# Optimization experiments

Measured on AMD Instinct MI355X. Metric: run time of the kernel, lower is better.

Reference implementation:

```python
import jax, jax.numpy as jnp
import numpy as np

N = 10000      # cells (nodes)
F_IN = 512     # genes (features)
H = 40         # hidden_dim
DEG = 16       # avg kNN degree
EPS = 1e-5     # GraphNorm eps


def gcn(x, W, b, src, dst, coef):
    # PyG GCNConv: transform then symmetric-normalized aggregate (+bias)
    h = x @ W                                   # [N, out]
    msg = h[src] * coef[:, None]                # [E, out]
    out = jax.ops.segment_sum(msg, dst, num_segments=N)
    return out + b


def graph_norm(x, weight, bias, alpha):
    # PyG GraphNorm over a single graph: mean/var across nodes, learnable mean scale
    mean = jnp.mean(x, axis=0, keepdims=True)
    shifted = x - alpha * mean
    var = jnp.mean(shifted * shifted, axis=0, keepdims=True)
    return weight * shifted * jax.lax.rsqrt(var + EPS) + bias


def setup_inputs() -> dict:
    key = jax.random.key(0)
    ks = jax.random.split(key, 8)
    x = jax.random.uniform(ks[0], (N, F_IN), dtype=jnp.float32)
    E = N * DEG
    src = jax.random.randint(ks[1], (E,), 0, N)
    dst = jax.random.randint(ks[2], (E,), 0, N)
    loop = jnp.arange(N)
    src = jnp.concatenate([src, loop])          # add self-loops (GCNConv default)
    dst = jnp.concatenate([dst, loop])

    def glorot(k, shape):
        lim = np.sqrt(6.0 / (shape[0] + shape[1])).astype(np.float32)
        return jax.random.uniform(k, shape, jnp.float32, -lim, lim)

    W1 = glorot(ks[3], (F_IN, H)); b1 = jnp.zeros((H,), jnp.float32)
    gn_w = jnp.ones((H,), jnp.float32)
    gn_b = jnp.zeros((H,), jnp.float32)
    gn_a = jnp.ones((H,), jnp.float32)          # mean_scale alpha
    Wm = glorot(ks[4], (H, F_IN)); bm = jnp.zeros((F_IN,), jnp.float32)
    Wd = glorot(ks[5], (H, F_IN)); bd = jnp.zeros((F_IN,), jnp.float32)
    Wp = glorot(ks[6], (H, F_IN)); bp = jnp.zeros((F_IN,), jnp.float32)
    return {"x": x, "src": src, "dst": dst, "W1": W1, "b1": b1,
            "gn_w": gn_w, "gn_b": gn_b, "gn_a": gn_a,
            "Wm": Wm, "bm": bm, "Wd": Wd, "bd": bd, "Wp": Wp, "bp": bp}


def reference(x, src, dst, W1, b1, gn_w, gn_b, gn_a, Wm, bm, Wd, bd, Wp, bp):
    # symmetric GCN normalization (self-loops already in edge list, so deg >= 1)
    deg = jax.ops.segment_sum(jnp.ones_like(src, dtype=x.dtype), dst, num_segments=N)
    dis = jax.lax.rsqrt(deg)
    coef = dis[src] * dis[dst]                  # [E]

    hidden = jax.nn.relu(graph_norm(gcn(x, W1, b1, src, dst, coef), gn_w, gn_b, gn_a))
    # Dropout(0.3) is identity at inference
    _mean = jnp.clip(jnp.exp(gcn(hidden, Wm, bm, src, dst, coef)), 1e-5, 1e6)
    _disp = jnp.clip(jax.nn.softplus(gcn(hidden, Wd, bd, src, dst, coef)), 1e-4, 1e4)
    _pi = jax.nn.sigmoid(gcn(hidden, Wp, bp, src, dst, coef))
    return (_mean, _disp, _pi)
```

## Files before the change

### kernel.cpp

```cpp
#include <hip/hip_runtime.h>
#include <math.h>

#define NN 10000
#define FIN 512
#define HD 40
#define GEPS 1e-5f

#define ZI4 ((2 * NN + 2 * HD) / 4)
#define MM1_BLOCKS ((NN + 15) / 16)
#define ZERO_BLOCKS ((ZI4 + 255) / 256)
#define CVT_BLOCKS ((3 * 32 * 3 * 64 + 255) / 256)

typedef _Float16 h4 __attribute__((ext_vector_type(4)));
typedef float f4 __attribute__((ext_vector_type(4)));

__global__ void k_hist(const int* __restrict__ dst, int* __restrict__ cnt, int E) {
    int e = blockIdx.x * blockDim.x + threadIdx.x;
    if (e < E) atomicAdd(&cnt[dst[e]], 1);
}

__global__ __launch_bounds__(1024) void k_scan(const int* __restrict__ cnt,
                                               int* __restrict__ rowstart,
                                               float* __restrict__ dis) {
    __shared__ int lds[1024];
    const int t = threadIdx.x;
    const int start = t * 16;
    int4 c[4];
    int s = 0;
    if (start < NN) {
#pragma unroll
        for (int q = 0; q < 4; ++q) {
            c[q] = *(const int4*)(cnt + start + q * 4);
            s += c[q].x + c[q].y + c[q].z + c[q].w;
        }
    }
    lds[t] = s;
    __syncthreads();
    for (int off = 1; off < 1024; off <<= 1) {
        int v = (t >= off) ? lds[t - off] : 0;
        __syncthreads();
        lds[t] += v;
        __syncthreads();
    }
    if (start < NN) {
        int run = lds[t] - s;
#pragma unroll
        for (int q = 0; q < 4; ++q) {
            int4 rs; float4 dv;
            rs.x = run; dv.x = rsqrtf((float)c[q].x); run += c[q].x;
            rs.y = run; dv.y = rsqrtf((float)c[q].y); run += c[q].y;
            rs.z = run; dv.z = rsqrtf((float)c[q].z); run += c[q].z;
            rs.w = run; dv.w = rsqrtf((float)c[q].w); run += c[q].w;
            *(int4*)(rowstart + start + q * 4) = rs;
            *(float4*)(dis + start + q * 4) = dv;
        }
        if (start + 16 == NN) rowstart[NN] = run;
    }
}

__global__ void k_fill(const int* __restrict__ src, const int* __restrict__ dst,
                       const int* __restrict__ rowstart, int* __restrict__ cur,
                       const float* __restrict__ dis, int2* __restrict__ csr, int E) {
    int e = blockIdx.x * blockDim.x + threadIdx.x;
    if (e >= E) return;
    int s = src[e], d = dst[e];
    int pos = rowstart[d] + atomicAdd(&cur[d], 1);
    int2 v;
    v.x = s;
    v.y = __float_as_int(dis[s] * dis[d]);
    csr[pos] = v;
}

__global__ __launch_bounds__(256) void k_mm1z(const float* __restrict__ x,
                                              const float* __restrict__ W1,
                                              float* __restrict__ h1,
                                              int4* __restrict__ zbuf,
                                              const float* __restrict__ Wm,
                                              const float* __restrict__ Wd,
                                              const float* __restrict__ Wp,
                                              _Float16* __restrict__ Whf) {
    if (blockIdx.x >= MM1_BLOCKS + ZERO_BLOCKS) {
        int idx = (blockIdx.x - MM1_BLOCKS - ZERO_BLOCKS) * 256 + threadIdx.x;
        if (idx < 3 * 32 * 3 * 64) {
            int lane = idx & 63;
            int kk   = (idx >> 6) % 3;
            int ct   = ((idx >> 6) / 3) % 32;
            int z    = idx / (64 * 3 * 32);
            const float* W = (z == 0) ? Wm : (z == 1) ? Wd : Wp;
            int col = ct * 16 + (lane & 15);
            h4 v;
#pragma unroll
            for (int j = 0; j < 4; ++j) {
                int krow = kk * 16 + (lane >> 4) * 4 + j;
                v[j] = (krow < HD) ? (_Float16)W[(size_t)krow * FIN + col] : (_Float16)0.f;
            }
            *(h4*)(Whf + (size_t)idx * 4) = v;
        }
        return;
    }
    if (blockIdx.x >= MM1_BLOCKS) {
        int i = (blockIdx.x - MM1_BLOCKS) * 256 + threadIdx.x;
        if (i < ZI4) zbuf[i] = make_int4(0, 0, 0, 0);
        return;
    }
    __shared__ float red[256 * 41];
    const int tid = threadIdx.x;
    const int r = tid & 15;
    const int kg = tid >> 4;
    const int row = blockIdx.x * 16 + r;
    const int rowc = min(row, NN - 1);
    const float4* xr = (const float4*)(x + (size_t)rowc * FIN + kg * 32);
    float acc[HD];
#pragma unroll
    for (int c = 0; c < HD; ++c) acc[c] = 0.f;
#pragma unroll 2
    for (int q = 0; q < 8; ++q) {
        float4 xv = xr[q];
        const float* wbase = W1 + (size_t)(kg * 32 + q * 4) * HD;
#pragma unroll
        for (int kk = 0; kk < 4; ++kk) {
            float xs = (kk == 0) ? xv.x : (kk == 1) ? xv.y : (kk == 2) ? xv.z : xv.w;
#pragma unroll
            for (int c4 = 0; c4 < 10; ++c4) {
                float4 wv = *(const float4*)(wbase + kk * HD + c4 * 4);
                acc[c4 * 4 + 0] = fmaf(xs, wv.x, acc[c4 * 4 + 0]);
                acc[c4 * 4 + 1] = fmaf(xs, wv.y, acc[c4 * 4 + 1]);
                acc[c4 * 4 + 2] = fmaf(xs, wv.z, acc[c4 * 4 + 2]);
                acc[c4 * 4 + 3] = fmaf(xs, wv.w, acc[c4 * 4 + 3]);
            }
        }
    }
#pragma unroll
    for (int c = 0; c < HD; ++c) red[tid * 41 + c] = acc[c];
    __syncthreads();
    if (tid < 160) {
        int rr = tid / 10, c4 = tid % 10;
        float o0 = 0.f, o1 = 0.f, o2 = 0.f, o3 = 0.f;
#pragma unroll
        for (int kg2 = 0; kg2 < 16; ++kg2) {
            const float* p = &red[(kg2 * 16 + rr) * 41 + c4 * 4];
            o0 += p[0]; o1 += p[1]; o2 += p[2]; o3 += p[3];
        }
        int orow = blockIdx.x * 16 + rr;
        if (orow < NN)
            *(float4*)&h1[(size_t)orow * HD + c4 * 4] = make_float4(o0, o1, o2, o3);
    }
}

template <bool NORM>
__global__ __launch_bounds__(256) void k_gather(const int* __restrict__ rowstart,
                                                const int2* __restrict__ csr,
                                                const float* __restrict__ hin,
                                                const float* __restrict__ stats,
                                                const float* __restrict__ b1,
                                                const float* __restrict__ gw,
                                                const float* __restrict__ gb,
                                                const float* __restrict__ ga,
                                                float* __restrict__ aggout_f,
                                                _Float16* __restrict__ aggout_h) {
    __shared__ float4 part[256];
    __shared__ float csc[2 * HD];
    const int t = threadIdx.x;
    if (NORM) {
        if (t < HD) {
            float m   = stats[t] * (1.0f / NN);
            float ex2 = stats[HD + t] * (1.0f / NN);
            float a   = ga[t];
            float var = ex2 - 2.0f * a * m * m + a * a * m * m;
            float sc  = gw[t] * rsqrtf(var + GEPS);
            csc[t]      = sc;
            csc[HD + t] = sc * (b1[t] - a * m) + gb[t];
        }
        __syncthreads();
    }
    const int slot = blockIdx.x * 128 + (t & 127);
    const int half = t >> 7;
    float4 acc = make_float4(0.f, 0.f, 0.f, 0.f);
    if (slot < NN * 10) {
        const int n = slot / 10, c4 = slot % 10;
        const int j0 = rowstart[n], j1 = rowstart[n + 1];
        const int mid = j0 + ((j1 - j0 + 1) >> 1);
        const int ja = half ? mid : j0;
        const int jb = half ? j1 : mid;
        float4 sc, sh;
        if (NORM) {
            sc = ((const float4*)csc)[c4];
            sh = ((const float4*)csc)[10 + c4];
        }
        for (int j = ja; j < jb; j += 8) {
            const int jm = jb - 1;
            int2 e[8];
#pragma unroll
            for (int q = 0; q < 8; ++q) e[q] = csr[min(j + q, jm)];
            float4 v[8];
#pragma unroll
            for (int q = 0; q < 8; ++q)
                v[q] = *(const float4*)&hin[(size_t)e[q].x * HD + c4 * 4];
#pragma unroll
            for (int q = 0; q < 8; ++q) {
                float cf = (j + q < jb) ? __int_as_float(e[q].y) : 0.f;
                if (NORM) {
                    v[q].x = fmaxf(fmaf(sc.x, v[q].x, sh.x), 0.f);
                    v[q].y = fmaxf(fmaf(sc.y, v[q].y, sh.y), 0.f);
                    v[q].z = fmaxf(fmaf(sc.z, v[q].z, sh.z), 0.f);
                    v[q].w = fmaxf(fmaf(sc.w, v[q].w, sh.w), 0.f);
                }
                acc.x = fmaf(v[q].x, cf, acc.x);
                acc.y = fmaf(v[q].y, cf, acc.y);
                acc.z = fmaf(v[q].z, cf, acc.z);
                acc.w = fmaf(v[q].w, cf, acc.w);
            }
        }
    }
    part[t] = acc;
    __syncthreads();
    if (half == 0 && slot < NN * 10) {
        const int n = slot / 10, c4 = slot % 10;
        float4 p2 = part[t + 128];
        acc.x += p2.x; acc.y += p2.y; acc.z += p2.z; acc.w += p2.w;
        if (NORM) {
            h4 hv = { (_Float16)acc.x, (_Float16)acc.y, (_Float16)acc.z, (_Float16)acc.w };
            *(h4*)(aggout_h + (size_t)n * 48 + c4 * 4) = hv;
            if (c4 == 0) {
                h4 zv = { (_Float16)0.f, (_Float16)0.f, (_Float16)0.f, (_Float16)0.f };
                *(h4*)(aggout_h + (size_t)n * 48 + 40) = zv;
                *(h4*)(aggout_h + (size_t)n * 48 + 44) = zv;
            }
        } else {
            ((float4*)aggout_f)[slot] = acc;
        }
    }
}

__global__ __launch_bounds__(256) void k_stats(const float* __restrict__ agg1,
                                               const float* __restrict__ b1,
                                               float* __restrict__ stats) {
    __shared__ float s0[HD], s1[HD];
    if (threadIdx.x < HD) { s0[threadIdx.x] = 0.f; s1[threadIdx.x] = 0.f; }
    __syncthreads();
    const int gid = blockIdx.x * 256 + threadIdx.x;
    const int c4 = gid % 10;
    float4 bv = ((const float4*)b1)[c4];
    float4 a0 = make_float4(0.f, 0.f, 0.f, 0.f);
    float4 a1 = a0;
    for (int i4 = gid; i4 < NN * 10; i4 += 80 * 256) {
        float4 v = ((const float4*)agg1)[i4];
        v.x += bv.x; v.y += bv.y; v.z += bv.z; v.w += bv.w;
        a0.x += v.x; a0.y += v.y; a0.z += v.z; a0.w += v.w;
        a1.x = fmaf(v.x, v.x, a1.x);
        a1.y = fmaf(v.y, v.y, a1.y);
        a1.z = fmaf(v.z, v.z, a1.z);
        a1.w = fmaf(v.w, v.w, a1.w);
    }
    atomicAdd(&s0[c4 * 4 + 0], a0.x); atomicAdd(&s0[c4 * 4 + 1], a0.y);
    atomicAdd(&s0[c4 * 4 + 2], a0.z); atomicAdd(&s0[c4 * 4 + 3], a0.w);
    atomicAdd(&s1[c4 * 4 + 0], a1.x); atomicAdd(&s1[c4 * 4 + 1], a1.y);
    atomicAdd(&s1[c4 * 4 + 2], a1.z); atomicAdd(&s1[c4 * 4 + 3], a1.w);
    __syncthreads();
    if (threadIdx.x < HD) {
        atomicAdd(&stats[threadIdx.x], s0[threadIdx.x]);
        atomicAdd(&stats[HD + threadIdx.x], s1[threadIdx.x]);
    }
}

__device__ __forceinline__ float activate_rt(float z, int act) {
    if (act == 0) {
        return fminf(fmaxf(__expf(z), 1e-5f), 1e6f);
    } else if (act == 1) {
        float sp = fmaxf(z, 0.0f) + __logf(1.0f + __expf(-fabsf(z)));
        return fminf(fmaxf(sp, 1e-4f), 1e4f);
    }
    return __fdividef(1.0f, 1.0f + __expf(-z));
}

__global__ __launch_bounds__(256) void k_heads3m(const _Float16* __restrict__ agghh,
                                                 const _Float16* __restrict__ Whf,
                                                 const float* __restrict__ bm,
                                                 const float* __restrict__ bd,
                                                 const float* __restrict__ bp,
                                                 float* __restrict__ out) {
    const int z = blockIdx.z;
    const float* bias = (z == 0) ? bm : (z == 1) ? bd : bp;
    float* o = out + (size_t)z * NN * FIN;

    const int lane = threadIdx.x & 63;
    const int wv   = threadIdx.x >> 6;
    const int rowbase = blockIdx.x * 16;
    const int r16  = lane & 15;
    const int kgrp = lane >> 4;

    const _Float16* arow = agghh + (size_t)(rowbase + r16) * 48 + kgrp * 4;
    h4 g0 = *(const h4*)(arow);
    h4 g1 = *(const h4*)(arow + 16);
    h4 g2 = *(const h4*)(arow + 32);

    const int grow = rowbase + r16;
    float* orow = o + (size_t)grow * FIN;

#pragma unroll
    for (int i = 0; i < 8; ++i) {
        const int ct = wv * 8 + i;
        const _Float16* wb = Whf + ((size_t)(z * 32 + ct) * 3) * 256 + lane * 4;
        h4 w0 = *(const h4*)(wb);
        h4 w1 = *(const h4*)(wb + 256);
        h4 w2 = *(const h4*)(wb + 512);
        f4 acc = {0.f, 0.f, 0.f, 0.f};
        acc = __builtin_amdgcn_mfma_f32_16x16x16f16(w0, g0, acc, 0, 0, 0);
        acc = __builtin_amdgcn_mfma_f32_16x16x16f16(w1, g1, acc, 0, 0, 0);
        acc = __builtin_amdgcn_mfma_f32_16x16x16f16(w2, g2, acc, 0, 0, 0);
        const int col0 = ct * 16 + kgrp * 4;
        float4 bv = *(const float4*)&bias[col0];
        float4 ov;
        ov.x = activate_rt(acc[0] + bv.x, z);
        ov.y = activate_rt(acc[1] + bv.y, z);
        ov.z = activate_rt(acc[2] + bv.z, z);
        ov.w = activate_rt(acc[3] + bv.w, z);
        *(float4*)(orow + col0) = ov;
    }
}

extern "C" void kernel_launch(void* const* d_in, const int* in_sizes, int n_in,
                              void* d_out, int out_size, void* d_ws, size_t ws_size,
                              hipStream_t stream) {
    const float* x   = (const float*)d_in[0];
    const int*   src = (const int*)d_in[1];
    const int*   dst = (const int*)d_in[2];
    const float* W1  = (const float*)d_in[3];
    const float* b1  = (const float*)d_in[4];
    const float* gnw = (const float*)d_in[5];
    const float* gnb = (const float*)d_in[6];
    const float* gna = (const float*)d_in[7];
    const float* Wm  = (const float*)d_in[8];
    const float* bm  = (const float*)d_in[9];
    const float* Wd  = (const float*)d_in[10];
    const float* bd  = (const float*)d_in[11];
    const float* Wp  = (const float*)d_in[12];
    const float* bp  = (const float*)d_in[13];
    const int E = in_sizes[1];

    float*     ws       = (float*)d_ws;
    float*     h1       = ws;
    float*     agg1     = h1 + (size_t)NN * HD;
    int*       cnt      = (int*)(agg1 + (size_t)NN * HD);
    int*       cur      = cnt + NN;
    float*     stats    = (float*)(cur + NN);
    float*     dis      = stats + 2 * HD;
    int*       rowstart = (int*)(dis + NN);
    int2*      csr      = (int2*)(rowstart + NN + 2);
    _Float16*  Whf      = (_Float16*)(csr + E);
    _Float16*  agghh    = (_Float16*)h1;
    float*     out      = (float*)d_out;

    k_mm1z<<<MM1_BLOCKS + ZERO_BLOCKS + CVT_BLOCKS, 256, 0, stream>>>(
        x, W1, h1, (int4*)cnt, Wm, Wd, Wp, Whf);
    k_hist<<<(E + 255) / 256, 256, 0, stream>>>(dst, cnt, E);
    k_scan<<<1, 1024, 0, stream>>>(cnt, rowstart, dis);
    k_fill<<<(E + 255) / 256, 256, 0, stream>>>(src, dst, rowstart, cur, dis, csr, E);
    const int gblocks = (NN * 10 + 127) / 128;
    k_gather<false><<<gblocks, 256, 0, stream>>>(rowstart, csr, h1, nullptr,
                                                 nullptr, nullptr, nullptr, nullptr,
                                                 agg1, nullptr);
    k_stats<<<80, 256, 0, stream>>>(agg1, b1, stats);
    k_gather<true><<<gblocks, 256, 0, stream>>>(rowstart, csr, agg1, stats,
                                                b1, gnw, gnb, gna,
                                                nullptr, agghh);
    dim3 hgrid(MM1_BLOCKS, 1, 3);
    k_heads3m<<<hgrid, 256, 0, stream>>>(agghh, Whf, bm, bd, bp, out);
}
```

Before: 110.3 us.

## Fuse GraphNorm stats into first gather and second gather into heads GEMM

Folds the column sum and sum-of-squares reduction into the first aggregation kernel using LDS atomics, removing the separate stats pass over agg1. It also merges the normalized second aggregation with the three MFMA output heads: each 512-thread block gathers 16 rows into shared fp16 and then computes all three heads for them. This removes two launches and the global round trip of the fp16 hidden buffer. In exchange, the gather phase runs on only 320 of 512 threads, the grid has far fewer blocks, and the stats kernel now does many more shared atomics.

```diff
diff --git a/kernel.cpp b/kernel.cpp
--- a/kernel.cpp
+++ b/kernel.cpp
@@ -147,32 +147,17 @@
     }
 }
 
-template <bool NORM>
-__global__ __launch_bounds__(256) void k_gather(const int* __restrict__ rowstart,
-                                                const int2* __restrict__ csr,
-                                                const float* __restrict__ hin,
-                                                const float* __restrict__ stats,
-                                                const float* __restrict__ b1,
-                                                const float* __restrict__ gw,
-                                                const float* __restrict__ gb,
-                                                const float* __restrict__ ga,
-                                                float* __restrict__ aggout_f,
-                                                _Float16* __restrict__ aggout_h) {
+__global__ __launch_bounds__(256) void k_gather1s(const int* __restrict__ rowstart,
+                                                  const int2* __restrict__ csr,
+                                                  const float* __restrict__ hin,
+                                                  const float* __restrict__ b1,
+                                                  float* __restrict__ agg1,
+                                                  float* __restrict__ stats) {
     __shared__ float4 part[256];
-    __shared__ float csc[2 * HD];
+    __shared__ float s0[HD], s1[HD];
     const int t = threadIdx.x;
-    if (NORM) {
-        if (t < HD) {
-            float m   = stats[t] * (1.0f / NN);
-            float ex2 = stats[HD + t] * (1.0f / NN);
-            float a   = ga[t];
-            float var = ex2 - 2.0f * a * m * m + a * a * m * m;
-            float sc  = gw[t] * rsqrtf(var + GEPS);
-            csc[t]      = sc;
-            csc[HD + t] = sc * (b1[t] - a * m) + gb[t];
-        }
-        __syncthreads();
-    }
+    if (t < HD) { s0[t] = 0.f; s1[t] = 0.f; }
+    __syncthreads();
     const int slot = blockIdx.x * 128 + (t & 127);
     const int half = t >> 7;
     float4 acc = make_float4(0.f, 0.f, 0.f, 0.f);
@@ -182,11 +167,6 @@
         const int mid = j0 + ((j1 - j0 + 1) >> 1);
         const int ja = half ? mid : j0;
         const int jb = half ? j1 : mid;
-        float4 sc, sh;
-        if (NORM) {
-            sc = ((const float4*)csc)[c4];
-            sh = ((const float4*)csc)[10 + c4];
-        }
         for (int j = ja; j < jb; j += 8) {
             const int jm = jb - 1;
             int2 e[8];
@@ -199,12 +179,6 @@
 #pragma unroll
             for (int q = 0; q < 8; ++q) {
                 float cf = (j + q < jb) ? __int_as_float(e[q].y) : 0.f;
-                if (NORM) {
-                    v[q].x = fmaxf(fmaf(sc.x, v[q].x, sh.x), 0.f);
-                    v[q].y = fmaxf(fmaf(sc.y, v[q].y, sh.y), 0.f);
-                    v[q].z = fmaxf(fmaf(sc.z, v[q].z, sh.z), 0.f);
-                    v[q].w = fmaxf(fmaf(sc.w, v[q].w, sh.w), 0.f);
-                }
                 acc.x = fmaf(v[q].x, cf, acc.x);
                 acc.y = fmaf(v[q].y, cf, acc.y);
                 acc.z = fmaf(v[q].z, cf, acc.z);
@@ -215,51 +189,21 @@
     part[t] = acc;
     __syncthreads();
     if (half == 0 && slot < NN * 10) {
-        const int n = slot / 10, c4 = slot % 10;
+        const int c4 = slot % 10;
         float4 p2 = part[t + 128];
         acc.x += p2.x; acc.y += p2.y; acc.z += p2.z; acc.w += p2.w;
-        if (NORM) {
-            h4 hv = { (_Float16)acc.x, (_Float16)acc.y, (_Float16)acc.z, (_Float16)acc.w };
-            *(h4*)(aggout_h + (size_t)n * 48 + c4 * 4) = hv;
-            if (c4 == 0) {
-                h4 zv = { (_Float16)0.f, (_Float16)0.f, (_Float16)0.f, (_Float16)0.f };
-                *(h4*)(aggout_h + (size_t)n * 48 + 40) = zv;
-                *(h4*)(aggout_h + (size_t)n * 48 + 44) = zv;
-            }
-        } else {
-            ((float4*)aggout_f)[slot] = acc;
-        }
-    }
-}
-
-__global__ __launch_bounds__(256) void k_stats(const float* __restrict__ agg1,
-                                               const float* __restrict__ b1,
-                                               float* __restrict__ stats) {
-    __shared__ float s0[HD], s1[HD];
-    if (threadIdx.x < HD) { s0[threadIdx.x] = 0.f; s1[threadIdx.x] = 0.f; }
-    __syncthreads();
-    const int gid = blockIdx.x * 256 + threadIdx.x;
-    const int c4 = gid % 10;
-    float4 bv = ((const float4*)b1)[c4];
-    float4 a0 = make_float4(0.f, 0.f, 0.f, 0.f);
-    float4 a1 = a0;
-    for (int i4 = gid; i4 < NN * 10; i4 += 80 * 256) {
-        float4 v = ((const float4*)agg1)[i4];
-        v.x += bv.x; v.y += bv.y; v.z += bv.z; v.w += bv.w;
-        a0.x += v.x; a0.y += v.y; a0.z += v.z; a0.w += v.w;
-        a1.x = fmaf(v.x, v.x, a1.x);
-        a1.y = fmaf(v.y, v.y, a1.y);
-        a1.z = fmaf(v.z, v.z, a1.z);
-        a1.w = fmaf(v.w, v.w, a1.w);
-    }
-    atomicAdd(&s0[c4 * 4 + 0], a0.x); atomicAdd(&s0[c4 * 4 + 1], a0.y);
-    atomicAdd(&s0[c4 * 4 + 2], a0.z); atomicAdd(&s0[c4 * 4 + 3], a0.w);
-    atomicAdd(&s1[c4 * 4 + 0], a1.x); atomicAdd(&s1[c4 * 4 + 1], a1.y);
-    atomicAdd(&s1[c4 * 4 + 2], a1.z); atomicAdd(&s1[c4 * 4 + 3], a1.w);
-    __syncthreads();
-    if (threadIdx.x < HD) {
-        atomicAdd(&stats[threadIdx.x], s0[threadIdx.x]);
-        atomicAdd(&stats[HD + threadIdx.x], s1[threadIdx.x]);
+        ((float4*)agg1)[slot] = acc;
+        float4 bv = ((const float4*)b1)[c4];
+        float vx = acc.x + bv.x, vy = acc.y + bv.y, vz = acc.z + bv.z, vw = acc.w + bv.w;
+        atomicAdd(&s0[c4 * 4 + 0], vx); atomicAdd(&s0[c4 * 4 + 1], vy);
+        atomicAdd(&s0[c4 * 4 + 2], vz); atomicAdd(&s0[c4 * 4 + 3], vw);
+        atomicAdd(&s1[c4 * 4 + 0], vx * vx); atomicAdd(&s1[c4 * 4 + 1], vy * vy);
+        atomicAdd(&s1[c4 * 4 + 2], vz * vz); atomicAdd(&s1[c4 * 4 + 3], vw * vw);
+    }
+    __syncthreads();
+    if (t < HD) {
+        atomicAdd(&stats[t], s0[t]);
+        atomicAdd(&stats[HD + t], s1[t]);
     }
 }
 
@@ -273,49 +217,119 @@
     return __fdividef(1.0f, 1.0f + __expf(-z));
 }
 
-__global__ __launch_bounds__(256) void k_heads3m(const _Float16* __restrict__ agghh,
-                                                 const _Float16* __restrict__ Whf,
-                                                 const float* __restrict__ bm,
-                                                 const float* __restrict__ bd,
-                                                 const float* __restrict__ bp,
-                                                 float* __restrict__ out) {
-    const int z = blockIdx.z;
-    const float* bias = (z == 0) ? bm : (z == 1) ? bd : bp;
-    float* o = out + (size_t)z * NN * FIN;
-
-    const int lane = threadIdx.x & 63;
-    const int wv   = threadIdx.x >> 6;
+__global__ __launch_bounds__(512) void k_gheads(const int* __restrict__ rowstart,
+                                                const int2* __restrict__ csr,
+                                                const float* __restrict__ agg1,
+                                                const float* __restrict__ stats,
+                                                const float* __restrict__ b1,
+                                                const float* __restrict__ gw,
+                                                const float* __restrict__ gb,
+                                                const float* __restrict__ ga,
+                                                const _Float16* __restrict__ Whf,
+                                                const float* __restrict__ bm,
+                                                const float* __restrict__ bd,
+                                                const float* __restrict__ bp,
+                                                float* __restrict__ out) {
+    __shared__ float csc[2 * HD];
+    __shared__ float4 part[320];
+    __shared__ _Float16 aggh_s[16 * 48];
+    const int t = threadIdx.x;
     const int rowbase = blockIdx.x * 16;
+
+    if (t < HD) {
+        float m   = stats[t] * (1.0f / NN);
+        float ex2 = stats[HD + t] * (1.0f / NN);
+        float a   = ga[t];
+        float var = ex2 - 2.0f * a * m * m + a * a * m * m;
+        float sc  = gw[t] * rsqrtf(var + GEPS);
+        csc[t]      = sc;
+        csc[HD + t] = sc * (b1[t] - a * m) + gb[t];
+    }
+    __syncthreads();
+
+    float4 acc = make_float4(0.f, 0.f, 0.f, 0.f);
+    if (t < 320) {
+        const int s = (t < 160) ? t : t - 160;
+        const int half = (t < 160) ? 0 : 1;
+        const int row = s / 10, c4 = s % 10;
+        const int n = rowbase + row;
+        const int j0 = rowstart[n], j1 = rowstart[n + 1];
+        const int mid = j0 + ((j1 - j0 + 1) >> 1);
+        const int ja = half ? mid : j0;
+        const int jb = half ? j1 : mid;
+        float4 sc = ((const float4*)csc)[c4];
+        float4 sh = ((const float4*)csc)[10 + c4];
+        for (int j = ja; j < jb; j += 8) {
+            const int jm = jb - 1;
+            int2 e[8];
+#pragma unroll
+            for (int q = 0; q < 8; ++q) e[q] = csr[min(j + q, jm)];
+            float4 v[8];
+#pragma unroll
+            for (int q = 0; q < 8; ++q)
+                v[q] = *(const float4*)&agg1[(size_t)e[q].x * HD + c4 * 4];
+#pragma unroll
+            for (int q = 0; q < 8; ++q) {
+                float cf = (j + q < jb) ? __int_as_float(e[q].y) : 0.f;
+                v[q].x = fmaxf(fmaf(sc.x, v[q].x, sh.x), 0.f);
+                v[q].y = fmaxf(fmaf(sc.y, v[q].y, sh.y), 0.f);
+                v[q].z = fmaxf(fmaf(sc.z, v[q].z, sh.z), 0.f);
+                v[q].w = fmaxf(fmaf(sc.w, v[q].w, sh.w), 0.f);
+                acc.x = fmaf(v[q].x, cf, acc.x);
+                acc.y = fmaf(v[q].y, cf, acc.y);
+                acc.z = fmaf(v[q].z, cf, acc.z);
+                acc.w = fmaf(v[q].w, cf, acc.w);
+            }
+        }
+        part[t] = acc;
+    }
+    __syncthreads();
+    if (t < 160) {
+        const int row = t / 10, c4 = t % 10;
+        float4 p2 = part[t + 160];
+        acc.x += p2.x; acc.y += p2.y; acc.z += p2.z; acc.w += p2.w;
+        h4 hv = { (_Float16)acc.x, (_Float16)acc.y, (_Float16)acc.z, (_Float16)acc.w };
+        *(h4*)(aggh_s + row * 48 + c4 * 4) = hv;
+        if (c4 == 0) {
+            h4 zv = { (_Float16)0.f, (_Float16)0.f, (_Float16)0.f, (_Float16)0.f };
+            *(h4*)(aggh_s + row * 48 + 40) = zv;
+            *(h4*)(aggh_s + row * 48 + 44) = zv;
+        }
+    }
+    __syncthreads();
+
+    const int lane = t & 63;
+    const int wvi  = t >> 6;
     const int r16  = lane & 15;
     const int kgrp = lane >> 4;
-
-    const _Float16* arow = agghh + (size_t)(rowbase + r16) * 48 + kgrp * 4;
+    const _Float16* arow = aggh_s + r16 * 48 + kgrp * 4;
     h4 g0 = *(const h4*)(arow);
     h4 g1 = *(const h4*)(arow + 16);
     h4 g2 = *(const h4*)(arow + 32);
-
     const int grow = rowbase + r16;
-    float* orow = o + (size_t)grow * FIN;
-
-#pragma unroll
-    for (int i = 0; i < 8; ++i) {
-        const int ct = wv * 8 + i;
+
+#pragma unroll
+    for (int i = 0; i < 12; ++i) {
+        const int job = wvi * 12 + i;
+        const int z = job >> 5;
+        const int ct = job & 31;
+        const float* bias = (z == 0) ? bm : (z == 1) ? bd : bp;
         const _Float16* wb = Whf + ((size_t)(z * 32 + ct) * 3) * 256 + lane * 4;
         h4 w0 = *(const h4*)(wb);
         h4 w1 = *(const h4*)(wb + 256);
         h4 w2 = *(const h4*)(wb + 512);
-        f4 acc = {0.f, 0.f, 0.f, 0.f};
-        acc = __builtin_amdgcn_mfma_f32_16x16x16f16(w0, g0, acc, 0, 0, 0);
-        acc = __builtin_amdgcn_mfma_f32_16x16x16f16(w1, g1, acc, 0, 0, 0);
-        acc = __builtin_amdgcn_mfma_f32_16x16x16f16(w2, g2, acc, 0, 0, 0);
+        f4 a = {0.f, 0.f, 0.f, 0.f};
+        a = __builtin_amdgcn_mfma_f32_16x16x16f16(w0, g0, a, 0, 0, 0);
+        a = __builtin_amdgcn_mfma_f32_16x16x16f16(w1, g1, a, 0, 0, 0);
+        a = __builtin_amdgcn_mfma_f32_16x16x16f16(w2, g2, a, 0, 0, 0);
         const int col0 = ct * 16 + kgrp * 4;
         float4 bv = *(const float4*)&bias[col0];
         float4 ov;
-        ov.x = activate_rt(acc[0] + bv.x, z);
-        ov.y = activate_rt(acc[1] + bv.y, z);
-        ov.z = activate_rt(acc[2] + bv.z, z);
-        ov.w = activate_rt(acc[3] + bv.w, z);
-        *(float4*)(orow + col0) = ov;
+        ov.x = activate_rt(a[0] + bv.x, z);
+        ov.y = activate_rt(a[1] + bv.y, z);
+        ov.z = activate_rt(a[2] + bv.z, z);
+        ov.w = activate_rt(a[3] + bv.w, z);
+        *(float4*)(out + (size_t)z * NN * FIN + (size_t)grow * FIN + col0) = ov;
     }
 }
 
@@ -348,7 +362,6 @@
     int*       rowstart = (int*)(dis + NN);
     int2*      csr      = (int2*)(rowstart + NN + 2);
     _Float16*  Whf      = (_Float16*)(csr + E);
-    _Float16*  agghh    = (_Float16*)h1;
     float*     out      = (float*)d_out;
 
     k_mm1z<<<MM1_BLOCKS + ZERO_BLOCKS + CVT_BLOCKS, 256, 0, stream>>>(
@@ -357,13 +370,8 @@
     k_scan<<<1, 1024, 0, stream>>>(cnt, rowstart, dis);
     k_fill<<<(E + 255) / 256, 256, 0, stream>>>(src, dst, rowstart, cur, dis, csr, E);
     const int gblocks = (NN * 10 + 127) / 128;
-    k_gather<false><<<gblocks, 256, 0, stream>>>(rowstart, csr, h1, nullptr,
-                                                 nullptr, nullptr, nullptr, nullptr,
-                                                 agg1, nullptr);
-    k_stats<<<80, 256, 0, stream>>>(agg1, b1, stats);
-    k_gather<true><<<gblocks, 256, 0, stream>>>(rowstart, csr, agg1, stats,
-                                                b1, gnw, gnb, gna,
-                                                nullptr, agghh);
-    dim3 hgrid(MM1_BLOCKS, 1, 3);
-    k_heads3m<<<hgrid, 256, 0, stream>>>(agghh, Whf, bm, bd, bp, out);
-}
+    k_gather1s<<<gblocks, 256, 0, stream>>>(rowstart, csr, h1, b1, agg1, stats);
+    k_gheads<<<MM1_BLOCKS, 512, 0, stream>>>(rowstart, csr, agg1, stats,
+                                             b1, gnw, gnb, gna,
+                                             Whf, bm, bd, bp, out);
+}
```

New measurement: 125.5 us. 13.8% more time.

## Split gather edges four ways and fuse histogram into first matmul launch

Applied to the files above, without the earlier changes.

The gather kernels now split each (node, column-group) slot's edge list across four wavefronts instead of two, with a 4-way LDS reduction. The aim is more parallelism and latency hiding for short kNN rows. The histogram atomics move into the first-layer matmul launch so both run concurrently. Zeroing and weight conversion move into their own small preceding kernel, which is needed because the histogram depends on the zeroed counts. The cost is one extra launch, twice as many gather blocks, and a larger reduction.

```diff
diff --git a/kernel.cpp b/kernel.cpp
--- a/kernel.cpp
+++ b/kernel.cpp
@@ -14,9 +14,86 @@
 typedef _Float16 h4 __attribute__((ext_vector_type(4)));
 typedef float f4 __attribute__((ext_vector_type(4)));
 
-__global__ void k_hist(const int* __restrict__ dst, int* __restrict__ cnt, int E) {
-    int e = blockIdx.x * blockDim.x + threadIdx.x;
-    if (e < E) atomicAdd(&cnt[dst[e]], 1);
+__global__ __launch_bounds__(256) void k_zc(int4* __restrict__ zbuf,
+                                            const float* __restrict__ Wm,
+                                            const float* __restrict__ Wd,
+                                            const float* __restrict__ Wp,
+                                            _Float16* __restrict__ Whf) {
+    if (blockIdx.x < ZERO_BLOCKS) {
+        int i = blockIdx.x * 256 + threadIdx.x;
+        if (i < ZI4) zbuf[i] = make_int4(0, 0, 0, 0);
+        return;
+    }
+    int idx = (blockIdx.x - ZERO_BLOCKS) * 256 + threadIdx.x;
+    if (idx < 3 * 32 * 3 * 64) {
+        int lane = idx & 63;
+        int kk   = (idx >> 6) % 3;
+        int ct   = ((idx >> 6) / 3) % 32;
+        int z    = idx / (64 * 3 * 32);
+        const float* W = (z == 0) ? Wm : (z == 1) ? Wd : Wp;
+        int col = ct * 16 + (lane & 15);
+        h4 v;
+#pragma unroll
+        for (int j = 0; j < 4; ++j) {
+            int krow = kk * 16 + (lane >> 4) * 4 + j;
+            v[j] = (krow < HD) ? (_Float16)W[(size_t)krow * FIN + col] : (_Float16)0.f;
+        }
+        *(h4*)(Whf + (size_t)idx * 4) = v;
+    }
+}
+
+__global__ __launch_bounds__(256) void k_histmm1(const float* __restrict__ x,
+                                                 const float* __restrict__ W1,
+                                                 float* __restrict__ h1,
+                                                 const int* __restrict__ dst,
+                                                 int* __restrict__ cnt, int E) {
+    if (blockIdx.x >= MM1_BLOCKS) {
+        int e = (blockIdx.x - MM1_BLOCKS) * 256 + threadIdx.x;
+        if (e < E) atomicAdd(&cnt[dst[e]], 1);
+        return;
+    }
+    __shared__ float red[256 * 41];
+    const int tid = threadIdx.x;
+    const int r = tid & 15;
+    const int kg = tid >> 4;
+    const int row = blockIdx.x * 16 + r;
+    const int rowc = min(row, NN - 1);
+    const float4* xr = (const float4*)(x + (size_t)rowc * FIN + kg * 32);
+    float acc[HD];
+#pragma unroll
+    for (int c = 0; c < HD; ++c) acc[c] = 0.f;
+#pragma unroll 2
+    for (int q = 0; q < 8; ++q) {
+        float4 xv = xr[q];
+        const float* wbase = W1 + (size_t)(kg * 32 + q * 4) * HD;
+#pragma unroll
+        for (int kk = 0; kk < 4; ++kk) {
+            float xs = (kk == 0) ? xv.x : (kk == 1) ? xv.y : (kk == 2) ? xv.z : xv.w;
+#pragma unroll
+            for (int c4 = 0; c4 < 10; ++c4) {
+                float4 wv = *(const float4*)(wbase + kk * HD + c4 * 4);
+                acc[c4 * 4 + 0] = fmaf(xs, wv.x, acc[c4 * 4 + 0]);
+                acc[c4 * 4 + 1] = fmaf(xs, wv.y, acc[c4 * 4 + 1]);
+                acc[c4 * 4 + 2] = fmaf(xs, wv.z, acc[c4 * 4 + 2]);
+                acc[c4 * 4 + 3] = fmaf(xs, wv.w, acc[c4 * 4 + 3]);
+            }
+        }
+    }
+#pragma unroll
+    for (int c = 0; c < HD; ++c) red[tid * 41 + c] = acc[c];
+    __syncthreads();
+    if (tid < 160) {
+        int rr = tid / 10, c4 = tid % 10;
+        float o0 = 0.f, o1 = 0.f, o2 = 0.f, o3 = 0.f;
+#pragma unroll
+        for (int kg2 = 0; kg2 < 16; ++kg2) {
+            const float* p = &red[(kg2 * 16 + rr) * 41 + c4 * 4];
+            o0 += p[0]; o1 += p[1]; o2 += p[2]; o3 += p[3];
+        }
+        int orow = blockIdx.x * 16 + rr;
+        if (orow < NN)
+            *(float4*)&h1[(size_t)orow * HD + c4 * 4] = make_float4(o0, o1, o2, o3);
+    }
 }
 
 __global__ __launch_bounds__(1024) void k_scan(const int* __restrict__ cnt,
@@ -71,93 +148,17 @@
     csr[pos] = v;
 }
 
-__global__ __launch_bounds__(256) void k_mm1z(const float* __restrict__ x,
-                                              const float* __restrict__ W1,
-                                              float* __restrict__ h1,
-                                              int4* __restrict__ zbuf,
-                                              const float* __restrict__ Wm,
-                                              const float* __restrict__ Wd,
-                                              const float* __restrict__ Wp,
-                                              _Float16* __restrict__ Whf) {
-    if (blockIdx.x >= MM1_BLOCKS + ZERO_BLOCKS) {
-        int idx = (blockIdx.x - MM1_BLOCKS - ZERO_BLOCKS) * 256 + threadIdx.x;
-        if (idx < 3 * 32 * 3 * 64) {
-            int lane = idx & 63;
-            int kk   = (idx >> 6) % 3;
-            int ct   = ((idx >> 6) / 3) % 32;
-            int z    = idx / (64 * 3 * 32);
-            const float* W = (z == 0) ? Wm : (z == 1) ? Wd : Wp;
-            int col = ct * 16 + (lane & 15);
-            h4 v;
-#pragma unroll
-            for (int j = 0; j < 4; ++j) {
-                int krow = kk * 16 + (lane >> 4) * 4 + j;
-                v[j] = (krow < HD) ? (_Float16)W[(size_t)krow * FIN + col] : (_Float16)0.f;
-            }
-            *(h4*)(Whf + (size_t)idx * 4) = v;
-        }
-        return;
-    }
-    if (blockIdx.x >= MM1_BLOCKS) {
-        int i = (blockIdx.x - MM1_BLOCKS) * 256 + threadIdx.x;
-        if (i < ZI4) zbuf[i] = make_int4(0, 0, 0, 0);
-        return;
-    }
-    __shared__ float red[256 * 41];
-    const int tid = threadIdx.x;
-    const int r = tid & 15;
-    const int kg = tid >> 4;
-    const int row = blockIdx.x * 16 + r;
-    const int rowc = min(row, NN - 1);
-    const float4* xr = (const float4*)(x + (size_t)rowc * FIN + kg * 32);
-    float acc[HD];
-#pragma unroll
-    for (int c = 0; c < HD; ++c) acc[c] = 0.f;
-#pragma unroll 2
-    for (int q = 0; q < 8; ++q) {
-        float4 xv = xr[q];
-        const float* wbase = W1 + (size_t)(kg * 32 + q * 4) * HD;
-#pragma unroll
-        for (int kk = 0; kk < 4; ++kk) {
-            float xs = (kk == 0) ? xv.x : (kk == 1) ? xv.y : (kk == 2) ? xv.z : xv.w;
-#pragma unroll
-            for (int c4 = 0; c4 < 10; ++c4) {
-                float4 wv = *(const float4*)(wbase + kk * HD + c4 * 4);
-                acc[c4 * 4 + 0] = fmaf(xs, wv.x, acc[c4 * 4 + 0]);
-                acc[c4 * 4 + 1] = fmaf(xs, wv.y, acc[c4 * 4 + 1]);
-                acc[c4 * 4 + 2] = fmaf(xs, wv.z, acc[c4 * 4 + 2]);
-                acc[c4 * 4 + 3] = fmaf(xs, wv.w, acc[c4 * 4 + 3]);
-            }
-        }
-    }
-#pragma unroll
-    for (int c = 0; c < HD; ++c) red[tid * 41 + c] = acc[c];
-    __syncthreads();
-    if (tid < 160) {
-        int rr = tid / 10, c4 = tid % 10;
-        float o0 = 0.f, o1 = 0.f, o2 = 0.f, o3 = 0.f;
-#pragma unroll
-        for (int kg2 = 0; kg2 < 16; ++kg2) {
-            const float* p = &red[(kg2 * 16 + rr) * 41 + c4 * 4];
-            o0 += p[0]; o1 += p[1]; o2 += p[2]; o3 += p[3];
-        }
-        int orow = blockIdx.x * 16 + rr;
-        if (orow < NN)
-            *(float4*)&h1[(size_t)orow * HD + c4 * 4] = make_float4(o0, o1, o2, o3);
-    }
-}
-
 template <bool NORM>
-__global__ __launch_bounds__(256) void k_gather(const int* __restrict__ rowstart,
-                                                const int2* __restrict__ csr,
-                                                const float* __restrict__ hin,
-                                                const float* __restrict__ stats,
-                                                const float* __restrict__ b1,
-                                                const float* __restrict__ gw,
-                                                const float* __restrict__ gb,
-                                                const float* __restrict__ ga,
-                                                float* __restrict__ aggout_f,
-                                                _Float16* __restrict__ aggout_h) {
+__global__ __launch_bounds__(256) void k_gather4(const int* __restrict__ rowstart,
+                                                 const int2* __restrict__ csr,
+                                                 const float* __restrict__ hin,
+                                                 const float* __restrict__ stats,
+                                                 const float* __restrict__ b1,
+                                                 const float* __restrict__ gw,
+                                                 const float* __restrict__ gb,
+                                                 const float* __restrict__ ga,
+                                                 float* __restrict__ aggout_f,
+                                                 _Float16* __restrict__ aggout_h) {
     __shared__ float4 part[256];
     __shared__ float csc[2 * HD];
     const int t = threadIdx.x;
@@ -173,15 +174,15 @@
         }
         __syncthreads();
     }
-    const int slot = blockIdx.x * 128 + (t & 127);
-    const int half = t >> 7;
+    const int slot = blockIdx.x * 64 + (t & 63);
+    const int qtr  = t >> 6;
     float4 acc = make_float4(0.f, 0.f, 0.f, 0.f);
     if (slot < NN * 10) {
         const int n = slot / 10, c4 = slot % 10;
         const int j0 = rowstart[n], j1 = rowstart[n + 1];
-        const int mid = j0 + ((j1 - j0 + 1) >> 1);
-        const int ja = half ? mid : j0;
-        const int jb = half ? j1 : mid;
+        const int len = j1 - j0;
+        const int ja = j0 + ((len * qtr) >> 2);
+        const int jb = j0 + ((len * (qtr + 1)) >> 2);
         float4 sc, sh;
         if (NORM) {
             sc = ((const float4*)csc)[c4];
@@ -214,10 +215,13 @@
     }
     part[t] = acc;
     __syncthreads();
-    if (half == 0 && slot < NN * 10) {
+    if (qtr == 0 && slot < NN * 10) {
         const int n = slot / 10, c4 = slot % 10;
-        float4 p2 = part[t + 128];
-        acc.x += p2.x; acc.y += p2.y; acc.z += p2.z; acc.w += p2.w;
+        float4 p1 = part[t + 64], p2 = part[t + 128], p3 = part[t + 192];
+        acc.x += p1.x + p2.x + p3.x;
+        acc.y += p1.y + p2.y + p3.y;
+        acc.z += p1.z + p2.z + p3.z;
+        acc.w += p1.w + p2.w + p3.w;
         if (NORM) {
             h4 hv = { (_Float16)acc.x, (_Float16)acc.y, (_Float16)acc.z, (_Float16)acc.w };
             *(h4*)(aggout_h + (size_t)n * 48 + c4 * 4) = hv;
@@ -351,19 +355,19 @@
     _Float16*  agghh    = (_Float16*)h1;
     float*     out      = (float*)d_out;
 
-    k_mm1z<<<MM1_BLOCKS + ZERO_BLOCKS + CVT_BLOCKS, 256, 0, stream>>>(
-        x, W1, h1, (int4*)cnt, Wm, Wd, Wp, Whf);
-    k_hist<<<(E + 255) / 256, 256, 0, stream>>>(dst, cnt, E);
+    k_zc<<<ZERO_BLOCKS + CVT_BLOCKS, 256, 0, stream>>>((int4*)cnt, Wm, Wd, Wp, Whf);
+    const int histb = (E + 255) / 256;
+    k_histmm1<<<MM1_BLOCKS + histb, 256, 0, stream>>>(x, W1, h1, dst, cnt, E);
     k_scan<<<1, 1024, 0, stream>>>(cnt, rowstart, dis);
     k_fill<<<(E + 255) / 256, 256, 0, stream>>>(src, dst, rowstart, cur, dis, csr, E);
-    const int gblocks = (NN * 10 + 127) / 128;
-    k_gather<false><<<gblocks, 256, 0, stream>>>(rowstart, csr, h1, nullptr,
-                                                 nullptr, nullptr, nullptr, nullptr,
-                                                 agg1, nullptr);
+    const int gblocks4 = (NN * 10 + 63) / 64;
+    k_gather4<false><<<gblocks4, 256, 0, stream>>>(rowstart, csr, h1, nullptr,
+                                                   nullptr, nullptr, nullptr, nullptr,
+                                                   agg1, nullptr);
     k_stats<<<80, 256, 0, stream>>>(agg1, b1, stats);
-    k_gather<true><<<gblocks, 256, 0, stream>>>(rowstart, csr, agg1, stats,
-                                                b1, gnw, gnb, gna,
-                                                nullptr, agghh);
+    k_gather4<true><<<gblocks4, 256, 0, stream>>>(rowstart, csr, agg1, stats,
+                                                  b1, gnw, gnb, gna,
+                                                  nullptr, agghh);
     dim3 hgrid(MM1_BLOCKS, 1, 3);
     k_heads3m<<<hgrid, 256, 0, stream>>>(agghh, Whf, bm, bd, bp, out);
 }
```

New measurement: 105.4 us, median of 2. 1.05x faster.
